# Performance work log

Hardware: AMD Instinct MI355X
Metric: run time of the kernel (lower is better)

## Reference

```python
import jax, jax.numpy as jnp
import numpy as np

V, D, H, L, B, T = 50257, 1024, 1024, 2, 64, 32


def setup_inputs() -> dict:
    key = jax.random.key(0)
    ks = jax.random.split(key, 8)
    s = 0.05  # keep GRU/proj activations in a sane range
    return {
        "embedding": jax.random.normal(ks[0], (V, D), jnp.float32) * s,
        "w_ih": jax.random.normal(ks[1], (L, 3 * H, D), jnp.float32) * s,
        "w_hh": jax.random.normal(ks[2], (L, 3 * H, H), jnp.float32) * s,
        "b_ih": jax.random.normal(ks[3], (L, 3 * H), jnp.float32) * s,
        "b_hh": jax.random.normal(ks[4], (L, 3 * H), jnp.float32) * s,
        "w_proj": jax.random.normal(ks[5], (V, H), jnp.float32) * s,
        "b_proj": jax.random.normal(ks[6], (V,), jnp.float32) * s,
        "initial_hidden": jax.random.normal(ks[7], (L, B, H), jnp.float32),
        "max_name_len": T,
        "start_token": 1,
        "batch_size": B,
    }


def _gru_cell(x, h, wi, wh, bi, bh):
    # PyTorch GRU gate order: r, z, n
    gi = x @ wi.T + bi            # [B, 3H]
    gh = h @ wh.T + bh            # [B, 3H]
    ir, iz, inn = jnp.split(gi, 3, axis=-1)
    hr, hz, hn = jnp.split(gh, 3, axis=-1)
    r = jax.nn.sigmoid(ir + hr)
    z = jax.nn.sigmoid(iz + hz)
    n = jnp.tanh(inn + r * hn)
    return (1.0 - z) * n + z * h


def reference(embedding, w_ih, w_hh, b_ih, b_hh, w_proj, b_proj,
              initial_hidden, max_name_len, start_token, batch_size):
    n_layers = initial_hidden.shape[0]
    tok0 = jnp.full((batch_size,), start_token, dtype=jnp.int32)

    def step(carry, _):
        h, tok = carry                      # h: [L,B,H], tok: [B]
        x = embedding[tok]                  # [B,D]
        hs = []
        for l in range(n_layers):           # small fixed layer loop
            hl = _gru_cell(x, h[l], w_ih[l], w_hh[l], b_ih[l], b_hh[l])
            hs.append(hl)
            x = hl
        h_new = jnp.stack(hs)               # [L,B,H]
        logits = x @ w_proj.T + b_proj      # [B,V]
        logp = jax.nn.log_softmax(logits, axis=-1)
        nxt = jnp.argmax(logits, axis=-1)   # greedy sampling (top_k k=0 is a no-op)
        return (h_new, nxt), (logp, nxt)

    (_, _), (logps, toks) = jax.lax.scan(step, (initial_hidden, tok0), None,
                                          length=max_name_len)
    # [T,B,V] -> [B,T,V]; [T,B] -> [B,T]
    return jnp.transpose(logps, (1, 0, 2)), jnp.transpose(toks, (1, 0))
```

## Files before the change

kernel.cpp:

```cpp
#include <hip/hip_runtime.h>
#include <hip/hip_bf16.h>
#include <math.h>

typedef __attribute__((ext_vector_type(8))) short bf16x8;
typedef __attribute__((ext_vector_type(4))) float f32x4;

#define VOCAB 50257
#define VPAD  50304
#define NCT   (VPAD / 16)
#define DIM   1024
#define HID   1024
#define TH3   3072
#define NL    2
#define NB    64
#define RCH   16
#define KCS   8

__device__ __forceinline__ unsigned short bf16_rne(float f) {
    unsigned int u = __float_as_uint(f);
    unsigned int r = u + 0x7FFFu + ((u >> 16) & 1u);
    return (unsigned short)(r >> 16);
}
__device__ __forceinline__ void split1(float f, unsigned short& h, unsigned short& l) {
    unsigned short hb = bf16_rne(f);
    float fh = __uint_as_float(((unsigned int)hb) << 16);
    h = hb;
    l = bf16_rne(f - fh);
}

__device__ __forceinline__ size_t tpos(int r, int k) {
    int ct = r >> 4, colr = r & 15, kc = k >> 5, kg = (k >> 3) & 3, j = k & 7;
    return ((((size_t)ct * 32 + kc) * 64) + (kg * 16 + colr)) * 8 + j;
}


__global__ __launch_bounds__(256) void k_split_w(const float* __restrict__ W,
                                                 unsigned short* __restrict__ th,
                                                 unsigned short* __restrict__ tl,
                                                 int nrows, size_t total) {
    size_t idx = (size_t)blockIdx.x * 256 + threadIdx.x;
    if (idx >= total) return;
    int r = (int)(idx >> 10), k = (int)(idx & 1023);
    float v = (r < nrows) ? W[(size_t)r * 1024 + k] : 0.f;
    unsigned short h, l;
    split1(v, h, l);
    size_t p = tpos(r, k);
    th[p] = h;
    tl[p] = l;
}

__global__ __launch_bounds__(256) void k_init_t(const float* __restrict__ h0,
                                                const int* __restrict__ start_tok,
                                                float* hbuf, unsigned short* hth,
                                                unsigned short* htl, int* tok) {
    int idx = blockIdx.x * 256 + threadIdx.x;
    if (idx < NL * NB * HID) {
        float v = h0[idx];
        hbuf[idx] = v;
        int l = idx >> 16;
        int b = (idx >> 10) & 63, i = idx & 1023;
        unsigned short h, lo;
        split1(v, h, lo);
        size_t p = (size_t)l * 65536 + tpos(b, i);
        hth[p] = h;
        htl[p] = lo;
    }
    if (idx < NB) tok[idx] = start_tok[0];
}

__global__ __launch_bounds__(256) void k_prep_x_t(const float* __restrict__ emb,
                                                  const int* __restrict__ tok,
                                                  unsigned short* xth, unsigned short* xtl) {
    int idx = blockIdx.x * 256 + threadIdx.x;
    int b = idx >> 10, k = idx & 1023;
    float v = emb[(size_t)tok[b] * DIM + k];
    unsigned short h, l;
    split1(v, h, l);
    size_t p = tpos(b, k);
    xth[p] = h;
    xtl[p] = l;
}

__global__ __launch_bounds__(256) void k_mm_gru_t(const unsigned short* __restrict__ Axh,
                                                  const unsigned short* __restrict__ Axl,
                                                  const unsigned short* __restrict__ Ahh,
                                                  const unsigned short* __restrict__ Ahl,
                                                  const unsigned short* __restrict__ Wihh,
                                                  const unsigned short* __restrict__ Wihl,
                                                  const unsigned short* __restrict__ Whhh,
                                                  const unsigned short* __restrict__ Whhl,
                                                  float* __restrict__ gpart) {
    const int wav = threadIdx.x >> 6, lane = threadIdx.x & 63;
    const int ct0 = blockIdx.x * 8 + wav * 2;
    const int kc0 = blockIdx.y * 4;
    const int colr = lane & 15, kg = lane >> 4;
    for (int m = 0; m < 2; ++m) {
        const bf16x8* A8h = (const bf16x8*)(m ? Ahh : Axh);
        const bf16x8* A8l = (const bf16x8*)(m ? Ahl : Axl);
        const bf16x8* B8h = (const bf16x8*)(m ? Whhh : Wihh);
        const bf16x8* B8l = (const bf16x8*)(m ? Whhl : Wihl);
        f32x4 acc[2][4];
#pragma unroll
        for (int nt = 0; nt < 2; ++nt)
#pragma unroll
            for (int mt = 0; mt < 4; ++mt)
                acc[nt][mt] = (f32x4){0.f, 0.f, 0.f, 0.f};
        for (int kc = kc0; kc < kc0 + 4; ++kc) {
            bf16x8 bh0 = B8h[((size_t)(ct0 + 0) * 32 + kc) * 64 + lane];
            bf16x8 bl0 = B8l[((size_t)(ct0 + 0) * 32 + kc) * 64 + lane];
            bf16x8 bh1 = B8h[((size_t)(ct0 + 1) * 32 + kc) * 64 + lane];
            bf16x8 bl1 = B8l[((size_t)(ct0 + 1) * 32 + kc) * 64 + lane];
#pragma unroll
            for (int mt = 0; mt < 4; ++mt) {
                bf16x8 ah = A8h[(mt * 32 + kc) * 64 + lane];
                bf16x8 al = A8l[(mt * 32 + kc) * 64 + lane];
                acc[0][mt] = __builtin_amdgcn_mfma_f32_16x16x32_bf16(ah, bh0, acc[0][mt], 0, 0, 0);
                acc[0][mt] = __builtin_amdgcn_mfma_f32_16x16x32_bf16(al, bh0, acc[0][mt], 0, 0, 0);
                acc[0][mt] = __builtin_amdgcn_mfma_f32_16x16x32_bf16(ah, bl0, acc[0][mt], 0, 0, 0);
                acc[1][mt] = __builtin_amdgcn_mfma_f32_16x16x32_bf16(ah, bh1, acc[1][mt], 0, 0, 0);
                acc[1][mt] = __builtin_amdgcn_mfma_f32_16x16x32_bf16(al, bh1, acc[1][mt], 0, 0, 0);
                acc[1][mt] = __builtin_amdgcn_mfma_f32_16x16x32_bf16(ah, bl1, acc[1][mt], 0, 0, 0);
            }
        }
        float* out = gpart + (size_t)(blockIdx.y * 2 + m) * 64 * TH3;
#pragma unroll
        for (int nt = 0; nt < 2; ++nt)
#pragma unroll
            for (int mt = 0; mt < 4; ++mt)
#pragma unroll
                for (int r = 0; r < 4; ++r) {
                    int col = (ct0 + nt) * 16 + colr;
                    int row = mt * 16 + kg * 4 + r;
                    out[(size_t)row * TH3 + col] = acc[nt][mt][r];
                }
    }
}

__global__ __launch_bounds__(256) void k_gate_t(const float* __restrict__ gpart,
                                                const float* __restrict__ bih,
                                                const float* __restrict__ bhh,
                                                float* hbuf, unsigned short* hth,
                                                unsigned short* htl) {
    int idx = blockIdx.x * 256 + threadIdx.x;
    int b = idx >> 10, i = idx & 1023;
    float ir = bih[i], iz = bih[HID + i], in = bih[2 * HID + i];
    float hr = bhh[i], hz = bhh[HID + i], hn = bhh[2 * HID + i];
#pragma unroll
    for (int kc = 0; kc < KCS; ++kc) {
        const float* gi = gpart + ((size_t)(kc * 2 + 0) * 64 + b) * TH3;
        const float* gh = gpart + ((size_t)(kc * 2 + 1) * 64 + b) * TH3;
        ir += gi[i]; iz += gi[HID + i]; in += gi[2 * HID + i];
        hr += gh[i]; hz += gh[HID + i]; hn += gh[2 * HID + i];
    }
    float r = 1.f / (1.f + expf(-(ir + hr)));
    float z = 1.f / (1.f + expf(-(iz + hz)));
    float n = tanhf(in + r * hn);
    float hold = hbuf[idx];
    float hnew = (1.f - z) * n + z * hold;
    hbuf[idx] = hnew;
    unsigned short h, lo;
    split1(hnew, h, lo);
    size_t p = tpos(b, i);
    hth[p] = h;
    htl[p] = lo;
}

__global__ __launch_bounds__(256) void k_mm_proj_t(const unsigned short* __restrict__ Ah,
                                                   const unsigned short* __restrict__ Al,
                                                   const unsigned short* __restrict__ Bh,
                                                   const unsigned short* __restrict__ Bl,
                                                   const float* __restrict__ bp,
                                                   float* __restrict__ logits, int Vt) {
    const int wav = threadIdx.x >> 6, lane = threadIdx.x & 63;
    const int ct0 = blockIdx.x * 8 + wav * 2;
    const int colr = lane & 15, kg = lane >> 4;
    const bf16x8* A8h = (const bf16x8*)Ah;
    const bf16x8* A8l = (const bf16x8*)Al;
    const bf16x8* B8h = (const bf16x8*)Bh;
    const bf16x8* B8l = (const bf16x8*)Bl;
    f32x4 acc[2][4];
#pragma unroll
    for (int nt = 0; nt < 2; ++nt)
#pragma unroll
        for (int mt = 0; mt < 4; ++mt)
            acc[nt][mt] = (f32x4){0.f, 0.f, 0.f, 0.f};
    for (int kc = 0; kc < 32; ++kc) {
        bf16x8 bh0 = B8h[((size_t)(ct0 + 0) * 32 + kc) * 64 + lane];
        bf16x8 bl0 = B8l[((size_t)(ct0 + 0) * 32 + kc) * 64 + lane];
        bf16x8 bh1 = B8h[((size_t)(ct0 + 1) * 32 + kc) * 64 + lane];
        bf16x8 bl1 = B8l[((size_t)(ct0 + 1) * 32 + kc) * 64 + lane];
#pragma unroll
        for (int mt = 0; mt < 4; ++mt) {
            bf16x8 ah = A8h[(mt * 32 + kc) * 64 + lane];
            bf16x8 al = A8l[(mt * 32 + kc) * 64 + lane];
            acc[0][mt] = __builtin_amdgcn_mfma_f32_16x16x32_bf16(ah, bh0, acc[0][mt], 0, 0, 0);
            acc[0][mt] = __builtin_amdgcn_mfma_f32_16x16x32_bf16(al, bh0, acc[0][mt], 0, 0, 0);
            acc[0][mt] = __builtin_amdgcn_mfma_f32_16x16x32_bf16(ah, bl0, acc[0][mt], 0, 0, 0);
            acc[1][mt] = __builtin_amdgcn_mfma_f32_16x16x32_bf16(ah, bh1, acc[1][mt], 0, 0, 0);
            acc[1][mt] = __builtin_amdgcn_mfma_f32_16x16x32_bf16(al, bh1, acc[1][mt], 0, 0, 0);
            acc[1][mt] = __builtin_amdgcn_mfma_f32_16x16x32_bf16(ah, bl1, acc[1][mt], 0, 0, 0);
        }
    }
#pragma unroll
    for (int nt = 0; nt < 2; ++nt)
#pragma unroll
        for (int mt = 0; mt < 4; ++mt)
#pragma unroll
            for (int r = 0; r < 4; ++r) {
                int col = (ct0 + nt) * 16 + colr;
                int row = mt * 16 + kg * 4 + r;
                float bv = (col < Vt) ? bp[col] : 0.f;
                logits[(size_t)row * VPAD + col] = acc[nt][mt][r] + bv;
            }
}


__global__ __launch_bounds__(256) void k_init(const float* __restrict__ h0,
                                              const int* __restrict__ start_tok,
                                              float* hbuf, unsigned short* hhi,
                                              unsigned short* hlo, int* tok) {
    int idx = blockIdx.x * 256 + threadIdx.x;
    if (idx < NL * NB * HID) {
        float v = h0[idx];
        hbuf[idx] = v;
        split1(v, hhi[idx], hlo[idx]);
    }
    if (idx < NB) tok[idx] = start_tok[0];
}

__global__ __launch_bounds__(256) void k_prep_x(const float* __restrict__ emb,
                                                const int* __restrict__ tok,
                                                unsigned short* xhi, unsigned short* xlo) {
    int idx = blockIdx.x * 256 + threadIdx.x;
    int b = idx >> 10, k = idx & 1023;
    float v = emb[(size_t)tok[b] * DIM + k];
    split1(v, xhi[idx], xlo[idx]);
}

__device__ __forceinline__ void mm_wave(const unsigned short* __restrict__ Ahi,
                                        const unsigned short* __restrict__ Alo,
                                        const float* __restrict__ W,
                                        int Ntot, int col, int k0, int klen,
                                        f32x4* acc) {
    const int lane = threadIdx.x & 63;
    const int colr = lane & 15;
    const int kg   = lane >> 4;
    const int colc = col < Ntot ? col : Ntot - 1;
    const float* wrow = W + (size_t)colc * 1024;
    for (int k = k0; k < k0 + klen; k += 32) {
        int ka = k + kg * 8;
        float4 b0 = *(const float4*)(wrow + ka);
        float4 b1 = *(const float4*)(wrow + ka + 4);
        float bv[8] = {b0.x, b0.y, b0.z, b0.w, b1.x, b1.y, b1.z, b1.w};
        bf16x8 bhi, blo;
#pragma unroll
        for (int j = 0; j < 8; ++j) {
            unsigned short h, l;
            split1(bv[j], h, l);
            bhi[j] = (short)h;
            blo[j] = (short)l;
        }
#pragma unroll
        for (int mt = 0; mt < 4; ++mt) {
            const bf16x8 ahi = *(const bf16x8*)(Ahi + (((mt * 16 + colr) << 10) + ka));
            const bf16x8 alo = *(const bf16x8*)(Alo + (((mt * 16 + colr) << 10) + ka));
            acc[mt] = __builtin_amdgcn_mfma_f32_16x16x32_bf16(ahi, bhi, acc[mt], 0, 0, 0);
            acc[mt] = __builtin_amdgcn_mfma_f32_16x16x32_bf16(alo, bhi, acc[mt], 0, 0, 0);
            acc[mt] = __builtin_amdgcn_mfma_f32_16x16x32_bf16(ahi, blo, acc[mt], 0, 0, 0);
        }
    }
}

__global__ __launch_bounds__(256) void k_mm_gru(const unsigned short* __restrict__ Axhi,
                                                const unsigned short* __restrict__ Axlo,
                                                const unsigned short* __restrict__ Ahhi,
                                                const unsigned short* __restrict__ Ahlo,
                                                const float* __restrict__ Wih,
                                                const float* __restrict__ Whh,
                                                float* __restrict__ gpart) {
    const int mat = blockIdx.z;
    const int kc  = blockIdx.y;
    const int wav = threadIdx.x >> 6;
    const int lane = threadIdx.x & 63;
    const int col = blockIdx.x * 64 + wav * 16 + (lane & 15);
    const unsigned short* Ahi = mat ? Ahhi : Axhi;
    const unsigned short* Alo = mat ? Ahlo : Axlo;
    const float* W = mat ? Whh : Wih;
    f32x4 acc[4] = {{0.f,0.f,0.f,0.f},{0.f,0.f,0.f,0.f},{0.f,0.f,0.f,0.f},{0.f,0.f,0.f,0.f}};
    mm_wave(Ahi, Alo, W, TH3, col, kc * 512, 512, acc);
    float* out = gpart + (size_t)(mat * 2 + kc) * NB * TH3;
    const int kg = lane >> 4;
#pragma unroll
    for (int mt = 0; mt < 4; ++mt)
#pragma unroll
        for (int r = 0; r < 4; ++r)
            out[(size_t)(mt * 16 + kg * 4 + r) * TH3 + col] = acc[mt][r];
}

__global__ __launch_bounds__(256) void k_gate(const float* __restrict__ gpart,
                                              const float* __restrict__ bih,
                                              const float* __restrict__ bhh,
                                              float* hbuf, unsigned short* hhi,
                                              unsigned short* hlo) {
    int idx = blockIdx.x * 256 + threadIdx.x;
    int b = idx >> 10, i = idx & 1023;
    const float* g00 = gpart;
    const float* g01 = gpart + (size_t)1 * NB * TH3;
    const float* g10 = gpart + (size_t)2 * NB * TH3;
    const float* g11 = gpart + (size_t)3 * NB * TH3;
    size_t o = (size_t)b * TH3;
    float ir = g00[o + i]            + g01[o + i]            + bih[i];
    float iz = g00[o + HID + i]      + g01[o + HID + i]      + bih[HID + i];
    float in = g00[o + 2 * HID + i]  + g01[o + 2 * HID + i]  + bih[2 * HID + i];
    float hr = g10[o + i]            + g11[o + i]            + bhh[i];
    float hz = g10[o + HID + i]      + g11[o + HID + i]      + bhh[HID + i];
    float hn = g10[o + 2 * HID + i]  + g11[o + 2 * HID + i]  + bhh[2 * HID + i];
    float r = 1.f / (1.f + expf(-(ir + hr)));
    float z = 1.f / (1.f + expf(-(iz + hz)));
    float n = tanhf(in + r * hn);
    float hold = hbuf[idx];
    float hnew = (1.f - z) * n + z * hold;
    hbuf[idx] = hnew;
    split1(hnew, hhi[idx], hlo[idx]);
}

__global__ __launch_bounds__(256) void k_mm_proj(const unsigned short* __restrict__ Ahi,
                                                 const unsigned short* __restrict__ Alo,
                                                 const float* __restrict__ Wp,
                                                 const float* __restrict__ bp,
                                                 float* __restrict__ logits, int Vt) {
    const int wav = threadIdx.x >> 6;
    const int lane = threadIdx.x & 63;
    const int col = blockIdx.x * 64 + wav * 16 + (lane & 15);
    f32x4 acc[4] = {{0.f,0.f,0.f,0.f},{0.f,0.f,0.f,0.f},{0.f,0.f,0.f,0.f},{0.f,0.f,0.f,0.f}};
    mm_wave(Ahi, Alo, Wp, Vt, col, 0, 1024, acc);
    if (col < Vt) {
        float bv = bp[col];
        const int kg = lane >> 4;
#pragma unroll
        for (int mt = 0; mt < 4; ++mt)
#pragma unroll
            for (int r = 0; r < 4; ++r)
                logits[(size_t)(mt * 16 + kg * 4 + r) * Vt + col] = acc[mt][r] + bv;
    }
}


__global__ __launch_bounds__(256) void k_reduce(const float* __restrict__ logits,
                                                float* __restrict__ red, int Vt, int ldl) {
    const int b = blockIdx.y, ch = blockIdx.x, tid = threadIdx.x;
    const int cs = (Vt + RCH - 1) / RCH;
    const int v0 = ch * cs;
    const int v1 = min(v0 + cs, Vt);
    const float* row = logits + (size_t)b * ldl;
    float m = -INFINITY; int mi = 0;
    for (int v = v0 + tid; v < v1; v += 256) {
        float x = row[v];
        if (x > m) { m = x; mi = v; }
    }
    __shared__ float sm[256]; __shared__ int si[256]; __shared__ float ss[256];
    sm[tid] = m; si[tid] = mi;
    __syncthreads();
    for (int s = 128; s > 0; s >>= 1) {
        if (tid < s) {
            float vo = sm[tid + s]; int io = si[tid + s];
            if (vo > sm[tid] || (vo == sm[tid] && io < si[tid])) { sm[tid] = vo; si[tid] = io; }
        }
        __syncthreads();
    }
    float mb = sm[0];
    float acc = 0.f;
    for (int v = v0 + tid; v < v1; v += 256) acc += expf(row[v] - mb);
    ss[tid] = acc;
    __syncthreads();
    for (int s = 128; s > 0; s >>= 1) {
        if (tid < s) ss[tid] += ss[tid + s];
        __syncthreads();
    }
    if (tid == 0)
        ((float4*)red)[b * RCH + ch] = make_float4(mb, ss[0], (float)si[0], 0.f);
}

__global__ __launch_bounds__(256) void k_final(const float* __restrict__ logits,
                                               const float* __restrict__ red,
                                               float* __restrict__ out_logp,
                                               float* __restrict__ out_tok,
                                               int* __restrict__ toknext,
                                               int Vt, int ldl, int Tt, int t) {
    const int b = blockIdx.y, tid = threadIdx.x;
    float mg = -INFINITY, ig = 0.f;
#pragma unroll
    for (int c = 0; c < RCH; ++c) {
        float4 p = ((const float4*)red)[b * RCH + c];
        if (p.x > mg) { mg = p.x; ig = p.z; }
        else if (p.x == mg && p.z < ig) { ig = p.z; }
    }
    float sg = 0.f;
#pragma unroll
    for (int c = 0; c < RCH; ++c) {
        float4 p = ((const float4*)red)[b * RCH + c];
        sg += p.y * expf(p.x - mg);
    }
    float lse = mg + logf(sg);
    const float* row = logits + (size_t)b * ldl;
    float* orow = out_logp + ((size_t)b * Tt + t) * Vt;
    const int base = blockIdx.x * 2048;
#pragma unroll
    for (int j = 0; j < 8; ++j) {
        int v = base + tid + j * 256;
        if (v < Vt) orow[v] = row[v] - lse;
    }
    if (blockIdx.x == 0 && tid == 0) {
        toknext[b] = (int)ig;
        out_tok[(size_t)b * Tt + t] = ig;
    }
}

extern "C" void kernel_launch(void* const* d_in, const int* in_sizes, int n_in,
                              void* d_out, int out_size, void* d_ws, size_t ws_size,
                              hipStream_t stream) {
    const float* emb    = (const float*)d_in[0];
    const float* w_ih   = (const float*)d_in[1];
    const float* w_hh   = (const float*)d_in[2];
    const float* b_ih   = (const float*)d_in[3];
    const float* b_hh   = (const float*)d_in[4];
    const float* w_proj = (const float*)d_in[5];
    const float* b_proj = (const float*)d_in[6];
    const float* h0     = (const float*)d_in[7];
    const int*   start  = (const int*)d_in[9];

    const int Vt = in_sizes[5] / HID;
    const int Tt = (int)((size_t)out_size / ((size_t)NB * (Vt + 1)));

    float* out_logp = (float*)d_out;
    float* out_tok  = (float*)d_out + (size_t)NB * Tt * Vt;

    const size_t SZ_BPROJ = (size_t)NCT * 32 * 64 * 8 * 2;
    const size_t SZ_GRUW  = (size_t)(TH3 / 16) * 32 * 64 * 8 * 2;
    const size_t SZ_HT    = (size_t)65536 * 2;

    char* ws = (char*)d_ws;
    size_t used = 0;
    auto alloc = [&](size_t bytes) {
        char* p = ws + used;
        used += (bytes + 255) & ~(size_t)255;
        return p;
    };
    float* logits        = (float*)alloc((size_t)NB * VPAD * 4);
    unsigned short* bpjh = (unsigned short*)alloc(SZ_BPROJ);
    unsigned short* bpjl = (unsigned short*)alloc(SZ_BPROJ);
    unsigned short* gwh[4]; unsigned short* gwl[4];
    for (int i = 0; i < 4; ++i) {
        gwh[i] = (unsigned short*)alloc(SZ_GRUW);
        gwl[i] = (unsigned short*)alloc(SZ_GRUW);
    }
    unsigned short* xth = (unsigned short*)alloc(SZ_HT);
    unsigned short* xtl = (unsigned short*)alloc(SZ_HT);
    unsigned short* hth = (unsigned short*)alloc(NL * SZ_HT);
    unsigned short* htl = (unsigned short*)alloc(NL * SZ_HT);
    float* hbuf          = (float*)alloc((size_t)NL * NB * HID * 4);
    float* gpart         = (float*)alloc((size_t)KCS * 2 * 64 * TH3 * 4);
    float* red           = (float*)alloc((size_t)NB * RCH * 16);
    int* tok             = (int*)alloc(256);

    if (ws_size >= used) {
        k_split_w<<<(int)(((size_t)VPAD * 1024 + 255) / 256), 256, 0, stream>>>(
            w_proj, bpjh, bpjl, Vt, (size_t)VPAD * 1024);
        for (int l = 0; l < NL; ++l) {
            k_split_w<<<(TH3 * 1024 / 256), 256, 0, stream>>>(
                w_ih + (size_t)l * TH3 * DIM, gwh[l * 2 + 0], gwl[l * 2 + 0], TH3, (size_t)TH3 * 1024);
            k_split_w<<<(TH3 * 1024 / 256), 256, 0, stream>>>(
                w_hh + (size_t)l * TH3 * HID, gwh[l * 2 + 1], gwl[l * 2 + 1], TH3, (size_t)TH3 * 1024);
        }
        k_init_t<<<(NL * NB * HID + 255) / 256, 256, 0, stream>>>(h0, start, hbuf, hth, htl, tok);

        for (int t = 0; t < Tt; ++t) {
            k_prep_x_t<<<NB * DIM / 256, 256, 0, stream>>>(emb, tok, xth, xtl);
            for (int l = 0; l < NL; ++l) {
                const unsigned short* Axh = (l == 0) ? xth : hth;
                const unsigned short* Axl = (l == 0) ? xtl : htl;
                const unsigned short* Ahh = hth + (size_t)l * 65536;
                const unsigned short* Ahl = htl + (size_t)l * 65536;
                k_mm_gru_t<<<dim3(TH3 / 128, KCS), 256, 0, stream>>>(
                    Axh, Axl, Ahh, Ahl,
                    gwh[l * 2 + 0], gwl[l * 2 + 0], gwh[l * 2 + 1], gwl[l * 2 + 1], gpart);
                k_gate_t<<<NB * HID / 256, 256, 0, stream>>>(
                    gpart, b_ih + (size_t)l * TH3, b_hh + (size_t)l * TH3,
                    hbuf + (size_t)l * NB * HID, hth + (size_t)l * 65536, htl + (size_t)l * 65536);
            }
            k_mm_proj_t<<<VPAD / 128, 256, 0, stream>>>(
                hth + 65536, htl + 65536, bpjh, bpjl, b_proj, logits, Vt);
            k_reduce<<<dim3(RCH, NB), 256, 0, stream>>>(logits, red, Vt, VPAD);
            k_final<<<dim3((Vt + 2047) / 2048, NB), 256, 0, stream>>>(
                logits, red, out_logp, out_tok, tok, Vt, VPAD, Tt, t);
        }
    } else {
        char* w = (char*)d_ws;
        float* logitsF       = (float*)w;  w += (size_t)NB * Vt * 4;
        unsigned short* a0hi = (unsigned short*)w;  w += (size_t)NB * DIM * 2;
        unsigned short* a0lo = (unsigned short*)w;  w += (size_t)NB * DIM * 2;
        float* hbufF         = (float*)w;  w += (size_t)NL * NB * HID * 4;
        unsigned short* hhi  = (unsigned short*)w;  w += (size_t)NL * NB * HID * 2;
        unsigned short* hlo  = (unsigned short*)w;  w += (size_t)NL * NB * HID * 2;
        float* gpartF        = (float*)w;  w += (size_t)4 * NB * TH3 * 4;
        float* redF          = (float*)w;  w += (size_t)NB * RCH * 16;
        int* tokF            = (int*)w;    w += 256;

        k_init<<<(NL * NB * HID + 255) / 256, 256, 0, stream>>>(h0, start, hbufF, hhi, hlo, tokF);
        for (int t = 0; t < Tt; ++t) {
            k_prep_x<<<NB * DIM / 256, 256, 0, stream>>>(emb, tokF, a0hi, a0lo);
            for (int l = 0; l < NL; ++l) {
                const unsigned short* Axhi = (l == 0) ? a0hi : hhi;
                const unsigned short* Axlo = (l == 0) ? a0lo : hlo;
                const unsigned short* Ahhi = hhi + (size_t)l * NB * HID;
                const unsigned short* Ahlo = hlo + (size_t)l * NB * HID;
                k_mm_gru<<<dim3(TH3 / 64, 2, 2), 256, 0, stream>>>(
                    Axhi, Axlo, Ahhi, Ahlo,
                    w_ih + (size_t)l * TH3 * DIM, w_hh + (size_t)l * TH3 * HID, gpartF);
                k_gate<<<NB * HID / 256, 256, 0, stream>>>(
                    gpartF, b_ih + (size_t)l * TH3, b_hh + (size_t)l * TH3,
                    hbufF + (size_t)l * NB * HID, hhi + (size_t)l * NB * HID,
                    hlo + (size_t)l * NB * HID);
            }
            k_mm_proj<<<dim3((Vt + 63) / 64, 1, 1), 256, 0, stream>>>(
                hhi + (size_t)NB * HID, hlo + (size_t)NB * HID, w_proj, b_proj, logitsF, Vt);
            k_reduce<<<dim3(RCH, NB), 256, 0, stream>>>(logitsF, redF, Vt, Vt);
            k_final<<<dim3((Vt + 2047) / 2048, NB), 256, 0, stream>>>(
                logitsF, redF, out_logp, out_tok, tokF, Vt, Vt, Tt, t);
        }
    }
}
```

Before: 4.528 ms.

## Increase split-K parallelism in GRU and projection GEMMs, fuse bias into reduce

The GRU matmul grid now spans 16 K-splits and a separate z dimension for the input and hidden products, so each block does only two K-chunks and many more blocks run at once. The vocabulary projection is split along K into two halves written to partial buffers. A new reduce kernel sums the halves, adds the bias, writes the logits and computes the per-chunk max and sum-exp. This trades extra partial-sum memory traffic and a larger gate reduction for better GPU occupancy on small-batch GEMMs.

Result: faster. 4.121 ms (-9.0%).

```diff
diff --git a/kernel.cpp b/kernel.cpp
--- a/kernel.cpp
+++ b/kernel.cpp
@@ -14,7 +14,7 @@
 #define NL    2
 #define NB    64
 #define RCH   16
-#define KCS   8
+#define GKC   16
 
 __device__ __forceinline__ unsigned short bf16_rne(float f) {
     unsigned int u = __float_as_uint(f);
@@ -92,48 +92,49 @@
                                                   float* __restrict__ gpart) {
     const int wav = threadIdx.x >> 6, lane = threadIdx.x & 63;
     const int ct0 = blockIdx.x * 8 + wav * 2;
-    const int kc0 = blockIdx.y * 4;
+    const int kc0 = blockIdx.y * 2;
+    const int m = blockIdx.z;
     const int colr = lane & 15, kg = lane >> 4;
-    for (int m = 0; m < 2; ++m) {
-        const bf16x8* A8h = (const bf16x8*)(m ? Ahh : Axh);
-        const bf16x8* A8l = (const bf16x8*)(m ? Ahl : Axl);
-        const bf16x8* B8h = (const bf16x8*)(m ? Whhh : Wihh);
-        const bf16x8* B8l = (const bf16x8*)(m ? Whhl : Wihl);
-        f32x4 acc[2][4];
-#pragma unroll
-        for (int nt = 0; nt < 2; ++nt)
-#pragma unroll
-            for (int mt = 0; mt < 4; ++mt)
-                acc[nt][mt] = (f32x4){0.f, 0.f, 0.f, 0.f};
-        for (int kc = kc0; kc < kc0 + 4; ++kc) {
-            bf16x8 bh0 = B8h[((size_t)(ct0 + 0) * 32 + kc) * 64 + lane];
-            bf16x8 bl0 = B8l[((size_t)(ct0 + 0) * 32 + kc) * 64 + lane];
-            bf16x8 bh1 = B8h[((size_t)(ct0 + 1) * 32 + kc) * 64 + lane];
-            bf16x8 bl1 = B8l[((size_t)(ct0 + 1) * 32 + kc) * 64 + lane];
-#pragma unroll
-            for (int mt = 0; mt < 4; ++mt) {
-                bf16x8 ah = A8h[(mt * 32 + kc) * 64 + lane];
-                bf16x8 al = A8l[(mt * 32 + kc) * 64 + lane];
-                acc[0][mt] = __builtin_amdgcn_mfma_f32_16x16x32_bf16(ah, bh0, acc[0][mt], 0, 0, 0);
-                acc[0][mt] = __builtin_amdgcn_mfma_f32_16x16x32_bf16(al, bh0, acc[0][mt], 0, 0, 0);
-                acc[0][mt] = __builtin_amdgcn_mfma_f32_16x16x32_bf16(ah, bl0, acc[0][mt], 0, 0, 0);
-                acc[1][mt] = __builtin_amdgcn_mfma_f32_16x16x32_bf16(ah, bh1, acc[1][mt], 0, 0, 0);
-                acc[1][mt] = __builtin_amdgcn_mfma_f32_16x16x32_bf16(al, bh1, acc[1][mt], 0, 0, 0);
-                acc[1][mt] = __builtin_amdgcn_mfma_f32_16x16x32_bf16(ah, bl1, acc[1][mt], 0, 0, 0);
+    const bf16x8* A8h = (const bf16x8*)(m ? Ahh : Axh);
+    const bf16x8* A8l = (const bf16x8*)(m ? Ahl : Axl);
+    const bf16x8* B8h = (const bf16x8*)(m ? Whhh : Wihh);
+    const bf16x8* B8l = (const bf16x8*)(m ? Whhl : Wihl);
+    f32x4 acc[2][4];
+#pragma unroll
+    for (int nt = 0; nt < 2; ++nt)
+#pragma unroll
+        for (int mt = 0; mt < 4; ++mt)
+            acc[nt][mt] = (f32x4){0.f, 0.f, 0.f, 0.f};
+#pragma unroll
+    for (int i = 0; i < 2; ++i) {
+        int kc = kc0 + i;
+        bf16x8 bh0 = B8h[((size_t)(ct0 + 0) * 32 + kc) * 64 + lane];
+        bf16x8 bl0 = B8l[((size_t)(ct0 + 0) * 32 + kc) * 64 + lane];
+        bf16x8 bh1 = B8h[((size_t)(ct0 + 1) * 32 + kc) * 64 + lane];
+        bf16x8 bl1 = B8l[((size_t)(ct0 + 1) * 32 + kc) * 64 + lane];
+#pragma unroll
+        for (int mt = 0; mt < 4; ++mt) {
+            bf16x8 ah = A8h[(mt * 32 + kc) * 64 + lane];
+            bf16x8 al = A8l[(mt * 32 + kc) * 64 + lane];
+            acc[0][mt] = __builtin_amdgcn_mfma_f32_16x16x32_bf16(ah, bh0, acc[0][mt], 0, 0, 0);
+            acc[0][mt] = __builtin_amdgcn_mfma_f32_16x16x32_bf16(al, bh0, acc[0][mt], 0, 0, 0);
+            acc[0][mt] = __builtin_amdgcn_mfma_f32_16x16x32_bf16(ah, bl0, acc[0][mt], 0, 0, 0);
+            acc[1][mt] = __builtin_amdgcn_mfma_f32_16x16x32_bf16(ah, bh1, acc[1][mt], 0, 0, 0);
+            acc[1][mt] = __builtin_amdgcn_mfma_f32_16x16x32_bf16(al, bh1, acc[1][mt], 0, 0, 0);
+            acc[1][mt] = __builtin_amdgcn_mfma_f32_16x16x32_bf16(ah, bl1, acc[1][mt], 0, 0, 0);
+        }
+    }
+    float* out = gpart + (size_t)(m * GKC + blockIdx.y) * 64 * TH3;
+#pragma unroll
+    for (int nt = 0; nt < 2; ++nt)
+#pragma unroll
+        for (int mt = 0; mt < 4; ++mt)
+#pragma unroll
+            for (int r = 0; r < 4; ++r) {
+                int col = (ct0 + nt) * 16 + colr;
+                int row = mt * 16 + kg * 4 + r;
+                out[(size_t)row * TH3 + col] = acc[nt][mt][r];
             }
-        }
-        float* out = gpart + (size_t)(blockIdx.y * 2 + m) * 64 * TH3;
-#pragma unroll
-        for (int nt = 0; nt < 2; ++nt)
-#pragma unroll
-            for (int mt = 0; mt < 4; ++mt)
-#pragma unroll
-                for (int r = 0; r < 4; ++r) {
-                    int col = (ct0 + nt) * 16 + colr;
-                    int row = mt * 16 + kg * 4 + r;
-                    out[(size_t)row * TH3 + col] = acc[nt][mt][r];
-                }
-    }
 }
 
 __global__ __launch_bounds__(256) void k_gate_t(const float* __restrict__ gpart,
@@ -146,9 +147,9 @@
     float ir = bih[i], iz = bih[HID + i], in = bih[2 * HID + i];
     float hr = bhh[i], hz = bhh[HID + i], hn = bhh[2 * HID + i];
 #pragma unroll
-    for (int kc = 0; kc < KCS; ++kc) {
-        const float* gi = gpart + ((size_t)(kc * 2 + 0) * 64 + b) * TH3;
-        const float* gh = gpart + ((size_t)(kc * 2 + 1) * 64 + b) * TH3;
+    for (int kc = 0; kc < GKC; ++kc) {
+        const float* gi = gpart + ((size_t)kc * 64 + b) * TH3;
+        const float* gh = gpart + ((size_t)(GKC + kc) * 64 + b) * TH3;
         ir += gi[i]; iz += gi[HID + i]; in += gi[2 * HID + i];
         hr += gh[i]; hz += gh[HID + i]; hn += gh[2 * HID + i];
     }
@@ -169,10 +170,10 @@
                                                    const unsigned short* __restrict__ Al,
                                                    const unsigned short* __restrict__ Bh,
                                                    const unsigned short* __restrict__ Bl,
-                                                   const float* __restrict__ bp,
-                                                   float* __restrict__ logits, int Vt) {
+                                                   float* __restrict__ part) {
     const int wav = threadIdx.x >> 6, lane = threadIdx.x & 63;
     const int ct0 = blockIdx.x * 8 + wav * 2;
+    const int kc0 = blockIdx.y * 16;
     const int colr = lane & 15, kg = lane >> 4;
     const bf16x8* A8h = (const bf16x8*)Ah;
     const bf16x8* A8l = (const bf16x8*)Al;
@@ -184,7 +185,8 @@
 #pragma unroll
         for (int mt = 0; mt < 4; ++mt)
             acc[nt][mt] = (f32x4){0.f, 0.f, 0.f, 0.f};
-    for (int kc = 0; kc < 32; ++kc) {
+#pragma unroll 2
+    for (int kc = kc0; kc < kc0 + 16; ++kc) {
         bf16x8 bh0 = B8h[((size_t)(ct0 + 0) * 32 + kc) * 64 + lane];
         bf16x8 bl0 = B8l[((size_t)(ct0 + 0) * 32 + kc) * 64 + lane];
         bf16x8 bh1 = B8h[((size_t)(ct0 + 1) * 32 + kc) * 64 + lane];
@@ -201,6 +203,7 @@
             acc[1][mt] = __builtin_amdgcn_mfma_f32_16x16x32_bf16(ah, bl1, acc[1][mt], 0, 0, 0);
         }
     }
+    float* out = part + (size_t)blockIdx.y * NB * VPAD;
 #pragma unroll
     for (int nt = 0; nt < 2; ++nt)
 #pragma unroll
@@ -209,9 +212,83 @@
             for (int r = 0; r < 4; ++r) {
                 int col = (ct0 + nt) * 16 + colr;
                 int row = mt * 16 + kg * 4 + r;
-                float bv = (col < Vt) ? bp[col] : 0.f;
-                logits[(size_t)row * VPAD + col] = acc[nt][mt][r] + bv;
+                out[(size_t)row * VPAD + col] = acc[nt][mt][r];
             }
+}
+
+__global__ __launch_bounds__(256) void k_reduce2(const float* __restrict__ part,
+                                                 const float* __restrict__ bp,
+                                                 float* __restrict__ logits,
+                                                 float* __restrict__ red, int Vt) {
+    const int b = blockIdx.y, ch = blockIdx.x, tid = threadIdx.x;
+    const int cs = (Vt + RCH - 1) / RCH;
+    const int v0 = ch * cs;
+    const int v1 = min(v0 + cs, Vt);
+    const float* p0 = part + (size_t)b * VPAD;
+    const float* p1 = part + (size_t)(NB + b) * VPAD;
+    float* lrow = logits + (size_t)b * VPAD;
+    float m = -INFINITY; int mi = 0;
+    for (int v = v0 + tid; v < v1; v += 256) {
+        float x = p0[v] + p1[v] + bp[v];
+        lrow[v] = x;
+        if (x > m) { m = x; mi = v; }
+    }
+    __shared__ float sm[256]; __shared__ int si[256]; __shared__ float ss[256];
+    sm[tid] = m; si[tid] = mi;
+    __syncthreads();
+    for (int s = 128; s > 0; s >>= 1) {
+        if (tid < s) {
+            float vo = sm[tid + s]; int io = si[tid + s];
+            if (vo > sm[tid] || (vo == sm[tid] && io < si[tid])) { sm[tid] = vo; si[tid] = io; }
+        }
+        __syncthreads();
+    }
+    float mb = sm[0];
+    float acc = 0.f;
+    for (int v = v0 + tid; v < v1; v += 256) acc += expf(lrow[v] - mb);
+    ss[tid] = acc;
+    __syncthreads();
+    for (int s = 128; s > 0; s >>= 1) {
+        if (tid < s) ss[tid] += ss[tid + s];
+        __syncthreads();
+    }
+    if (tid == 0)
+        ((float4*)red)[b * RCH + ch] = make_float4(mb, ss[0], (float)si[0], 0.f);
+}
+
+__global__ __launch_bounds__(256) void k_final(const float* __restrict__ logits,
+                                               const float* __restrict__ red,
+                                               float* __restrict__ out_logp,
+                                               float* __restrict__ out_tok,
+                                               int* __restrict__ toknext,
+                                               int Vt, int ldl, int Tt, int t) {
+    const int b = blockIdx.y, tid = threadIdx.x;
+    float mg = -INFINITY, ig = 0.f;
+#pragma unroll
+    for (int c = 0; c < RCH; ++c) {
+        float4 p = ((const float4*)red)[b * RCH + c];
+        if (p.x > mg) { mg = p.x; ig = p.z; }
+        else if (p.x == mg && p.z < ig) { ig = p.z; }
+    }
+    float sg = 0.f;
+#pragma unroll
+    for (int c = 0; c < RCH; ++c) {
+        float4 p = ((const float4*)red)[b * RCH + c];
+        sg += p.y * expf(p.x - mg);
+    }
+    float lse = mg + logf(sg);
+    const float* row = logits + (size_t)b * ldl;
+    float* orow = out_logp + ((size_t)b * Tt + t) * Vt;
+    const int base = blockIdx.x * 2048;
+#pragma unroll
+    for (int j = 0; j < 8; ++j) {
+        int v = base + tid + j * 256;
+        if (v < Vt) orow[v] = row[v] - lse;
+    }
+    if (blockIdx.x == 0 && tid == 0) {
+        toknext[b] = (int)ig;
+        out_tok[(size_t)b * Tt + t] = ig;
+    }
 }
 
 
@@ -345,7 +422,6 @@
     }
 }
 
-
 __global__ __launch_bounds__(256) void k_reduce(const float* __restrict__ logits,
                                                 float* __restrict__ red, int Vt, int ldl) {
     const int b = blockIdx.y, ch = blockIdx.x, tid = threadIdx.x;
@@ -379,41 +455,6 @@
     }
     if (tid == 0)
         ((float4*)red)[b * RCH + ch] = make_float4(mb, ss[0], (float)si[0], 0.f);
-}
-
-__global__ __launch_bounds__(256) void k_final(const float* __restrict__ logits,
-                                               const float* __restrict__ red,
-                                               float* __restrict__ out_logp,
-                                               float* __restrict__ out_tok,
-                                               int* __restrict__ toknext,
-                                               int Vt, int ldl, int Tt, int t) {
-    const int b = blockIdx.y, tid = threadIdx.x;
-    float mg = -INFINITY, ig = 0.f;
-#pragma unroll
-    for (int c = 0; c < RCH; ++c) {
-        float4 p = ((const float4*)red)[b * RCH + c];
-        if (p.x > mg) { mg = p.x; ig = p.z; }
-        else if (p.x == mg && p.z < ig) { ig = p.z; }
-    }
-    float sg = 0.f;
-#pragma unroll
-    for (int c = 0; c < RCH; ++c) {
-        float4 p = ((const float4*)red)[b * RCH + c];
-        sg += p.y * expf(p.x - mg);
-    }
-    float lse = mg + logf(sg);
-    const float* row = logits + (size_t)b * ldl;
-    float* orow = out_logp + ((size_t)b * Tt + t) * Vt;
-    const int base = blockIdx.x * 2048;
-#pragma unroll
-    for (int j = 0; j < 8; ++j) {
-        int v = base + tid + j * 256;
-        if (v < Vt) orow[v] = row[v] - lse;
-    }
-    if (blockIdx.x == 0 && tid == 0) {
-        toknext[b] = (int)ig;
-        out_tok[(size_t)b * Tt + t] = ig;
-    }
 }
 
 extern "C" void kernel_launch(void* const* d_in, const int* in_sizes, int n_in,
@@ -438,6 +479,8 @@
     const size_t SZ_BPROJ = (size_t)NCT * 32 * 64 * 8 * 2;
     const size_t SZ_GRUW  = (size_t)(TH3 / 16) * 32 * 64 * 8 * 2;
     const size_t SZ_HT    = (size_t)65536 * 2;
+    const size_t SZ_GPART = (size_t)2 * GKC * 64 * TH3 * 4 > (size_t)2 * NB * VPAD * 4
+                          ? (size_t)2 * GKC * 64 * TH3 * 4 : (size_t)2 * NB * VPAD * 4;
 
     char* ws = (char*)d_ws;
     size_t used = 0;
@@ -459,7 +502,7 @@
     unsigned short* hth = (unsigned short*)alloc(NL * SZ_HT);
     unsigned short* htl = (unsigned short*)alloc(NL * SZ_HT);
     float* hbuf          = (float*)alloc((size_t)NL * NB * HID * 4);
-    float* gpart         = (float*)alloc((size_t)KCS * 2 * 64 * TH3 * 4);
+    float* gpart         = (float*)alloc(SZ_GPART);
     float* red           = (float*)alloc((size_t)NB * RCH * 16);
     int* tok             = (int*)alloc(256);
 
@@ -481,16 +524,16 @@
                 const unsigned short* Axl = (l == 0) ? xtl : htl;
                 const unsigned short* Ahh = hth + (size_t)l * 65536;
                 const unsigned short* Ahl = htl + (size_t)l * 65536;
-                k_mm_gru_t<<<dim3(TH3 / 128, KCS), 256, 0, stream>>>(
+                k_mm_gru_t<<<dim3(TH3 / 128, GKC, 2), 256, 0, stream>>>(
                     Axh, Axl, Ahh, Ahl,
                     gwh[l * 2 + 0], gwl[l * 2 + 0], gwh[l * 2 + 1], gwl[l * 2 + 1], gpart);
                 k_gate_t<<<NB * HID / 256, 256, 0, stream>>>(
                     gpart, b_ih + (size_t)l * TH3, b_hh + (size_t)l * TH3,
                     hbuf + (size_t)l * NB * HID, hth + (size_t)l * 65536, htl + (size_t)l * 65536);
             }
-            k_mm_proj_t<<<VPAD / 128, 256, 0, stream>>>(
-                hth + 65536, htl + 65536, bpjh, bpjl, b_proj, logits, Vt);
-            k_reduce<<<dim3(RCH, NB), 256, 0, stream>>>(logits, red, Vt, VPAD);
+            k_mm_proj_t<<<dim3(VPAD / 128, 2), 256, 0, stream>>>(
+                hth + 65536, htl + 65536, bpjh, bpjl, gpart);
+            k_reduce2<<<dim3(RCH, NB), 256, 0, stream>>>(gpart, b_proj, logits, red, Vt);
             k_final<<<dim3((Vt + 2047) / 2048, NB), 256, 0, stream>>>(
                 logits, red, out_logp, out_tok, tok, Vt, VPAD, Tt, t);
         }
```
